# Kernel optimization log

Hardware: AMD Instinct MI355X
Metric: run time of the kernel (lower is better)

Reference implementation:

```python
import jax, jax.numpy as jnp
import numpy as np

NUM_EMBEDDINGS = 1024
EMBEDDING_DIM = 256


def setup_inputs() -> dict:
    key = jax.random.key(0)
    k_in, k_w = jax.random.split(key)
    inputs = jax.random.normal(k_in, (32, EMBEDDING_DIM, 2048), dtype=jnp.float32)
    # nn.Embedding weight initialized uniform in [-1/K, 1/K]
    bound = 1.0 / NUM_EMBEDDINGS
    weight = jax.random.uniform(k_w, (NUM_EMBEDDINGS, EMBEDDING_DIM),
                                dtype=jnp.float32, minval=-bound, maxval=bound)
    return {"inputs": inputs, "weight": weight}


def reference(inputs, weight):
    B, D, T = inputs.shape
    # [B, D, T] -> [B*T, D]
    flat = jnp.transpose(inputs, (0, 2, 1)).reshape(-1, D)
    distances = (jnp.sum(flat * flat, axis=1, keepdims=True)
                 + jnp.sum(weight * weight, axis=1)
                 - 2.0 * flat @ weight.T)  # [N, K]
    encoding_indices = jnp.argmin(distances, axis=1)  # [N]
    # one-hot @ weight is just a gather
    quantized = weight[encoding_indices].reshape(B, T, D)  # [B, T, D]
    quantized = jnp.transpose(quantized, (0, 2, 1))  # [B, D, T]
    # straight-through estimator
    quantized = inputs + jax.lax.stop_gradient(quantized - inputs)
    return quantized, encoding_indices[:, None]
```

## Files before the change

### kernel.cpp

```cpp
#include <hip/hip_runtime.h>


#define VQ_B   32
#define VQ_D   256
#define VQ_T   2048
#define VQ_K   1024

typedef _Float16 f16x8 __attribute__((ext_vector_type(8)));
typedef _Float16 f16x4 __attribute__((ext_vector_type(4)));
typedef float    f32x4 __attribute__((ext_vector_type(4)));

#define GLOAD_LDS16(gaddr, laddr) \
  __builtin_amdgcn_global_load_lds((const __attribute__((address_space(1))) void*)(gaddr), \
                                   (__attribute__((address_space(3))) void*)(laddr), 16, 0, 0)

__global__ __launch_bounds__(256) void vq_wprep_kernel(
    const float* __restrict__ w, float* __restrict__ wnorm,
    _Float16* __restrict__ Wh, _Float16* __restrict__ Wl)
{
    __shared__ double ws_[16][16];
    const int tid = threadIdx.x;
    const int kk  = tid >> 4;
    const int dg  = tid & 15;
    const int k   = blockIdx.x * 16 + kk;
    const float* src = w + (size_t)k * VQ_D + dg * 16;
    double s = 0.0;
    #pragma unroll
    for (int q = 0; q < 4; ++q) {
        float4 v = *(const float4*)(src + q * 4);
        s += (double)v.x * v.x + (double)v.y * v.y
           + (double)v.z * v.z + (double)v.w * v.w;
        const float e4[4] = {v.x, v.y, v.z, v.w};
        f16x4 hv, lv;
        #pragma unroll
        for (int j = 0; j < 4; ++j) {
            const float es = e4[j] * 1024.0f;
            const _Float16 h = (_Float16)es;
            hv[j] = h;
            lv[j] = (_Float16)((es - (float)h) * 16777216.0f);
        }
        *(f16x4*)(Wh + (size_t)k * VQ_D + dg * 16 + q * 4) = hv;
        *(f16x4*)(Wl + (size_t)k * VQ_D + dg * 16 + q * 4) = lv;
    }
    ws_[kk][dg] = s;
    __syncthreads();
    if (dg == 0) {
        double acc = 0.0;
        #pragma unroll
        for (int g = 0; g < 16; ++g) acc += ws_[kk][g];
        wnorm[k] = (float)acc;
    }
}

__global__ __launch_bounds__(256, 2) void vq_mfma_kernel(
    const _Float16* __restrict__ Wh, const _Float16* __restrict__ Wl,
    const float* __restrict__ inp,
    const float* __restrict__ wnorm,
    const float* __restrict__ w,
    float* __restrict__ outq, float* __restrict__ outi)
{
    __shared__ alignas(16) char stg[2][32768];
    __shared__ double xs[2][128];
    const int tid  = threadIdx.x;
    const int lane = tid & 63;
    const int wv   = tid >> 6;
    const int m16  = lane & 15;
    const int quad = lane >> 4;
    const int wm   = wv & 1;
    const int wn   = wv >> 1;
    const int b    = blockIdx.x >> 4;
    const int tt0  = (blockIdx.x & 15) * 128;
    const long bt  = (long)b * VQ_T + tt0;

    const char* gp[8];
    #pragma unroll
    for (int i = 0; i < 8; ++i) {
        if (wv < 2) {
            const int hf = i >> 2, f = i & 3;
            const char* baseW = (const char*)((wv & 1) ? Wl : Wh);
            gp[i] = baseW + (size_t)(hf * 64 + f * 16 + m16) * 512 + quad * 16;
        } else {
            const int r  = (wv - 2) * 16 + i * 2 + (lane >> 5);
            const int sw = ((wv - 2) * 2 + (i >> 2)) * 2;
            gp[i] = (const char*)inp
                  + ((size_t)b * VQ_D + r) * (size_t)(VQ_T * 4)
                  + (size_t)(tt0 * 4)
                  + (size_t)(((lane & 31) ^ sw) * 16);
        }
    }
    auto advance = [&](int q) {
        if ((q & 7) == 7) {
            #pragma unroll
            for (int i = 0; i < 8; ++i)
                gp[i] += (wv < 2) ? (long)(65536 - 448) : (long)(-7) * 262144;
        } else {
            #pragma unroll
            for (int i = 0; i < 8; ++i)
                gp[i] += (wv < 2) ? 64L : 262144L;
        }
    };

    int tsw[4];
    #pragma unroll
    for (int f = 0; f < 4; ++f) {
        const int tl = wn * 64 + f * 16 + m16;
        tsw[f] = (((tl >> 2) ^ (quad * 2)) << 2) | (tl & 3);
    }

    const int xt_t  = tid & 127;
    const int xhalf = tid >> 7;
    double xacc = 0.0;
    float  xnr[4];

    float bestv[4] = {3.0e38f, 3.0e38f, 3.0e38f, 3.0e38f};
    int   besti[4] = {0, 0, 0, 0};
    f32x4 acch[4][4], accl[4][4];

    #pragma unroll
    for (int i = 0; i < 8; ++i)
        GLOAD_LDS16(gp[i], &stg[0][(wv * 8 + i) * 1024]);
    advance(0);

    for (int s = 0; s < 64; ++s) {
        const int cur = s & 1;
        if ((s & 7) == 0) {
            #pragma unroll
            for (int fm = 0; fm < 4; ++fm)
                #pragma unroll
                for (int fn = 0; fn < 4; ++fn) {
                    acch[fm][fn] = (f32x4){0.f, 0.f, 0.f, 0.f};
                    accl[fm][fn] = (f32x4){0.f, 0.f, 0.f, 0.f};
                }
        }
        __syncthreads();
        if (s < 63) {
            #pragma unroll
            for (int i = 0; i < 8; ++i)
                GLOAD_LDS16(gp[i], &stg[cur ^ 1][(wv * 8 + i) * 1024]);
            advance(s + 1);
        }

        const char*  base  = stg[cur];
        const float* xtile = (const float*)(base + 16384);

        f16x8 ah[4], al[4], bh[4], bl[4];
        #pragma unroll
        for (int f = 0; f < 4; ++f) {
            ah[f] = *(const f16x8*)(base + ((wm * 4 + f)) * 1024 + lane * 16);
            al[f] = *(const f16x8*)(base + ((8 + wm * 4 + f)) * 1024 + lane * 16);
        }
        #pragma unroll
        for (int f = 0; f < 4; ++f) {
            f16x8 hv, lv;
            #pragma unroll
            for (int j = 0; j < 8; ++j) {
                const float x = xtile[(quad * 8 + j) * 128 + tsw[f]];
                const _Float16 h = (_Float16)x;
                hv[j] = h;
                lv[j] = (_Float16)((x - (float)h) * 16777216.0f);
            }
            bh[f] = hv; bl[f] = lv;
        }

        #pragma unroll
        for (int fm = 0; fm < 4; ++fm)
            #pragma unroll
            for (int fn = 0; fn < 4; ++fn) {
                acch[fm][fn] = __builtin_amdgcn_mfma_f32_16x16x32_f16(
                    ah[fm], bh[fn], acch[fm][fn], 0, 0, 0);
                accl[fm][fn] = __builtin_amdgcn_mfma_f32_16x16x32_f16(
                    ah[fm], bl[fn], accl[fm][fn], 0, 0, 0);
                accl[fm][fn] = __builtin_amdgcn_mfma_f32_16x16x32_f16(
                    al[fm], bh[fn], accl[fm][fn], 0, 0, 0);
            }

        if (s < 8 && (s >> 2) == xhalf) {
            #pragma unroll
            for (int dd = 0; dd < 32; ++dd) {
                const float x = xtile[dd * 128 +
                    ((((xt_t >> 2) ^ ((dd >> 3) * 2)) << 2) | (xt_t & 3))];
                xacc += (double)x * (double)x;
            }
        }
        if (s == 7) {
            xs[xhalf][xt_t] = xacc;
            __syncthreads();
            #pragma unroll
            for (int fn = 0; fn < 4; ++fn) {
                const int tl = wn * 64 + fn * 16 + m16;
                xnr[fn] = (float)(xs[0][tl] + xs[1][tl]);
            }
        }

        if ((s & 7) == 7) {
            const int k0 = (s >> 3) * 128;
            #pragma unroll
            for (int fm = 0; fm < 4; ++fm) {
                #pragma unroll
                for (int r = 0; r < 4; ++r) {
                    const int kg = k0 + wm * 64 + fm * 16 + quad * 4 + r;
                    const float wnk = wnorm[kg];
                    #pragma unroll
                    for (int fn = 0; fn < 4; ++fn) {
                        const float t1 = xnr[fn] + wnk;
                        const float d2 = (acch[fm][fn][r]
                                          + accl[fm][fn][r] * 5.9604644775390625e-8f)
                                         * 0.001953125f;
                        const float sc = t1 - d2;
                        if (sc < bestv[fn]) { bestv[fn] = sc; besti[fn] = kg; }
                    }
                }
            }
        }
    }

    float rv[4]; int ri[4];
    #pragma unroll
    for (int fn = 0; fn < 4; ++fn) {
        float bv = bestv[fn]; int bi = besti[fn];
        #pragma unroll
        for (int mask = 16; mask <= 32; mask <<= 1) {
            const float ov = __shfl_xor(bv, mask, 64);
            const int   oi = __shfl_xor(bi, mask, 64);
            if (ov < bv || (ov == bv && oi < bi)) { bv = ov; bi = oi; }
        }
        rv[fn] = bv; ri[fn] = bi;
    }

    __syncthreads();
    float* sv = (float*)stg[0];
    int*   si = (int*)(stg[0] + 1024);
    if (quad == 0) {
        #pragma unroll
        for (int fn = 0; fn < 4; ++fn) {
            const int tl = wn * 64 + fn * 16 + m16;
            sv[wm * 128 + tl] = rv[fn];
            si[wm * 128 + tl] = ri[fn];
        }
    }
    __syncthreads();
    if (tid < 128) {
        const float v0 = sv[tid], v1 = sv[128 + tid];
        const int   i0 = si[tid], i1 = si[128 + tid];
        const int   bi = (v1 < v0 || (v1 == v0 && i1 < i0)) ? i1 : i0;
        si[tid] = bi;
        outi[bt + tid] = (float)bi;
    }
    __syncthreads();

    {
        const int t  = tid & 127;
        const int dh = tid >> 7;
        const int bi = si[t];
        const float* wrow = w + (size_t)bi * VQ_D + dh * 128;
        float* obase = outq + ((size_t)b * VQ_D + (size_t)dh * 128) * VQ_T + tt0 + t;
        #pragma unroll 4
        for (int dd = 0; dd < 128; dd += 4) {
            float4 v = *(const float4*)(wrow + dd);
            obase[(size_t)(dd + 0) * VQ_T] = v.x;
            obase[(size_t)(dd + 1) * VQ_T] = v.y;
            obase[(size_t)(dd + 2) * VQ_T] = v.z;
            obase[(size_t)(dd + 3) * VQ_T] = v.w;
        }
    }
}

extern "C" void kernel_launch(void* const* d_in, const int* in_sizes, int n_in,
                              void* d_out, int out_size, void* d_ws, size_t ws_size,
                              hipStream_t stream) {
    const float* inp = (const float*)d_in[0];
    const float* w   = (const float*)d_in[1];
    float* outq  = (float*)d_out;
    float* outi  = outq + (size_t)VQ_B * VQ_D * VQ_T;

    float*    wnorm = (float*)d_ws;
    _Float16* Wh    = (_Float16*)(wnorm + VQ_K);
    _Float16* Wl    = Wh + (size_t)VQ_K * VQ_D;

    vq_wprep_kernel<<<dim3(VQ_K / 16), dim3(256), 0, stream>>>(w, wnorm, Wh, Wl);
    vq_mfma_kernel<<<dim3(VQ_B * (VQ_T / 128)), dim3(256), 0, stream>>>(
        Wh, Wl, inp, wnorm, w, outq, outi);
}
```

Before: 251.8 us.

## Keep pre-split input tile resident in LDS and stream codebook through registers

The input tile for 64 tokens is loaded from global memory once, split into fp16 hi/lo parts and kept resident in LDS, with the token norm computed in the same pass. Before, the fp32 input tile was re-fetched from global memory and re-split on every step for each of the 8 codebook groups. The fp16 codebook is now streamed through registers into LDS with a register prefetch, replacing the async global-to-LDS double buffer. The token tile is halved and the grid doubled, which lowers MFMA reuse per step, doubles total codebook reads from L2 and adds a second barrier per step.

```diff
diff --git a/kernel.cpp b/kernel.cpp
--- a/kernel.cpp
+++ b/kernel.cpp
@@ -9,10 +9,6 @@
 typedef _Float16 f16x8 __attribute__((ext_vector_type(8)));
 typedef _Float16 f16x4 __attribute__((ext_vector_type(4)));
 typedef float    f32x4 __attribute__((ext_vector_type(4)));
-
-#define GLOAD_LDS16(gaddr, laddr) \
-  __builtin_amdgcn_global_load_lds((const __attribute__((address_space(1))) void*)(gaddr), \
-                                   (__attribute__((address_space(3))) void*)(laddr), 16, 0, 0)
 
 __global__ __launch_bounds__(256) void vq_wprep_kernel(
     const float* __restrict__ w, float* __restrict__ wnorm,
@@ -59,8 +55,11 @@
     const float* __restrict__ w,
     float* __restrict__ outq, float* __restrict__ outi)
 {
-    __shared__ alignas(16) char stg[2][32768];
-    __shared__ double xs[2][128];
+    __shared__ alignas(16) char lds[81920];
+    char* Xh = lds;
+    char* Xl = lds + 32768;
+    char* Wb = lds + 65536;
+
     const int tid  = threadIdx.x;
     const int lane = tid & 63;
     const int wv   = tid >> 6;
@@ -68,104 +67,111 @@
     const int quad = lane >> 4;
     const int wm   = wv & 1;
     const int wn   = wv >> 1;
-    const int b    = blockIdx.x >> 4;
-    const int tt0  = (blockIdx.x & 15) * 128;
+    const int b    = blockIdx.x >> 5;
+    const int tt0  = (blockIdx.x & 31) * 64;
     const long bt  = (long)b * VQ_T + tt0;
 
-    const char* gp[8];
-    #pragma unroll
-    for (int i = 0; i < 8; ++i) {
-        if (wv < 2) {
-            const int hf = i >> 2, f = i & 3;
-            const char* baseW = (const char*)((wv & 1) ? Wl : Wh);
-            gp[i] = baseW + (size_t)(hf * 64 + f * 16 + m16) * 512 + quad * 16;
-        } else {
-            const int r  = (wv - 2) * 16 + i * 2 + (lane >> 5);
-            const int sw = ((wv - 2) * 2 + (i >> 2)) * 2;
-            gp[i] = (const char*)inp
-                  + ((size_t)b * VQ_D + r) * (size_t)(VQ_T * 4)
-                  + (size_t)(tt0 * 4)
-                  + (size_t)(((lane & 31) ^ sw) * 16);
-        }
-    }
-    auto advance = [&](int q) {
-        if ((q & 7) == 7) {
-            #pragma unroll
-            for (int i = 0; i < 8; ++i)
-                gp[i] += (wv < 2) ? (long)(65536 - 448) : (long)(-7) * 262144;
-        } else {
-            #pragma unroll
-            for (int i = 0; i < 8; ++i)
-                gp[i] += (wv < 2) ? 64L : 262144L;
-        }
-    };
-
-    int tsw[4];
-    #pragma unroll
-    for (int f = 0; f < 4; ++f) {
-        const int tl = wn * 64 + f * 16 + m16;
-        tsw[f] = (((tl >> 2) ^ (quad * 2)) << 2) | (tl & 3);
-    }
-
-    const int xt_t  = tid & 127;
-    const int xhalf = tid >> 7;
+    const int sel  = tid >> 7;
+    const int r128 = tid & 127;
+    const _Float16* wsrc = (sel ? Wl : Wh) + (size_t)r128 * VQ_D;
+    char* wdst = Wb + (sel * 8 + (r128 >> 6) * 4 + ((r128 >> 4) & 3)) * 1024
+               + (r128 & 15) * 16;
+
+    f16x8 wreg[4];
+    #pragma unroll
+    for (int q = 0; q < 4; ++q)
+        wreg[q] = *(const f16x8*)(wsrc + q * 8);
+
+    const int xt = m16 + wv * 16;
     double xacc = 0.0;
-    float  xnr[4];
-
-    float bestv[4] = {3.0e38f, 3.0e38f, 3.0e38f, 3.0e38f};
-    int   besti[4] = {0, 0, 0, 0};
-    f32x4 acch[4][4], accl[4][4];
-
-    #pragma unroll
-    for (int i = 0; i < 8; ++i)
-        GLOAD_LDS16(gp[i], &stg[0][(wv * 8 + i) * 1024]);
-    advance(0);
+    {
+        float xv[2][8];
+        const float* xp0 = inp + ((size_t)b * VQ_D + quad * 8) * VQ_T + tt0 + xt;
+        #pragma unroll
+        for (int j = 0; j < 8; ++j)
+            xv[0][j] = xp0[(size_t)j * VQ_T];
+        #pragma unroll
+        for (int c = 0; c < 8; ++c) {
+            if (c < 7) {
+                const float* xpn = inp
+                    + ((size_t)b * VQ_D + (c + 1) * 32 + quad * 8) * VQ_T
+                    + tt0 + xt;
+                #pragma unroll
+                for (int j = 0; j < 8; ++j)
+                    xv[(c + 1) & 1][j] = xpn[(size_t)j * VQ_T];
+            }
+            f16x8 hv, lv;
+            #pragma unroll
+            for (int j = 0; j < 8; ++j) {
+                const float x = xv[c & 1][j];
+                xacc += (double)x * (double)x;
+                const _Float16 h = (_Float16)x;
+                hv[j] = h;
+                lv[j] = (_Float16)((x - (float)h) * 16777216.0f);
+            }
+            const int off = ((c * 4 + quad) * 64 + xt) * 16;
+            *(f16x8*)(Xh + off) = hv;
+            *(f16x8*)(Xl + off) = lv;
+        }
+    }
+    xacc += __shfl_xor(xacc, 16, 64);
+    xacc += __shfl_xor(xacc, 32, 64);
+    {
+        float* xns = (float*)Wb;
+        if (quad == 0) xns[xt] = (float)xacc;
+    }
+    __syncthreads();
+    float xnr[2];
+    #pragma unroll
+    for (int f = 0; f < 2; ++f)
+        xnr[f] = ((const float*)Wb)[wn * 32 + f * 16 + m16];
+    __syncthreads();
+
+    float bestv[2] = {3.0e38f, 3.0e38f};
+    int   besti[2] = {0, 0};
+    f32x4 acch[4][2], accl[4][2];
 
     for (int s = 0; s < 64; ++s) {
-        const int cur = s & 1;
-        if ((s & 7) == 0) {
+        const int c = s & 7;
+        #pragma unroll
+        for (int q = 0; q < 4; ++q)
+            *(f16x8*)(wdst + q * 256) = wreg[q];
+        __syncthreads();
+        if (s < 63) {
+            const int s1  = s + 1;
+            const _Float16* src = wsrc
+                + (size_t)((s1 >> 3) * 128) * VQ_D + (s1 & 7) * 32;
+            #pragma unroll
+            for (int q = 0; q < 4; ++q)
+                wreg[q] = *(const f16x8*)(src + q * 8);
+        }
+
+        if (c == 0) {
             #pragma unroll
             for (int fm = 0; fm < 4; ++fm)
                 #pragma unroll
-                for (int fn = 0; fn < 4; ++fn) {
+                for (int fn = 0; fn < 2; ++fn) {
                     acch[fm][fn] = (f32x4){0.f, 0.f, 0.f, 0.f};
                     accl[fm][fn] = (f32x4){0.f, 0.f, 0.f, 0.f};
                 }
         }
-        __syncthreads();
-        if (s < 63) {
-            #pragma unroll
-            for (int i = 0; i < 8; ++i)
-                GLOAD_LDS16(gp[i], &stg[cur ^ 1][(wv * 8 + i) * 1024]);
-            advance(s + 1);
-        }
-
-        const char*  base  = stg[cur];
-        const float* xtile = (const float*)(base + 16384);
-
-        f16x8 ah[4], al[4], bh[4], bl[4];
-        #pragma unroll
-        for (int f = 0; f < 4; ++f) {
-            ah[f] = *(const f16x8*)(base + ((wm * 4 + f)) * 1024 + lane * 16);
-            al[f] = *(const f16x8*)(base + ((8 + wm * 4 + f)) * 1024 + lane * 16);
-        }
-        #pragma unroll
-        for (int f = 0; f < 4; ++f) {
-            f16x8 hv, lv;
-            #pragma unroll
-            for (int j = 0; j < 8; ++j) {
-                const float x = xtile[(quad * 8 + j) * 128 + tsw[f]];
-                const _Float16 h = (_Float16)x;
-                hv[j] = h;
-                lv[j] = (_Float16)((x - (float)h) * 16777216.0f);
-            }
-            bh[f] = hv; bl[f] = lv;
-        }
-
+
+        f16x8 ah[4], al[4], bh[2], bl[2];
+        #pragma unroll
+        for (int fm = 0; fm < 4; ++fm) {
+            ah[fm] = *(const f16x8*)(Wb + (wm * 4 + fm) * 1024 + lane * 16);
+            al[fm] = *(const f16x8*)(Wb + (8 + wm * 4 + fm) * 1024 + lane * 16);
+        }
+        #pragma unroll
+        for (int f = 0; f < 2; ++f) {
+            const int off = ((c * 4 + quad) * 64 + wn * 32 + f * 16 + m16) * 16;
+            bh[f] = *(const f16x8*)(Xh + off);
+            bl[f] = *(const f16x8*)(Xl + off);
+        }
         #pragma unroll
         for (int fm = 0; fm < 4; ++fm)
             #pragma unroll
-            for (int fn = 0; fn < 4; ++fn) {
+            for (int fn = 0; fn < 2; ++fn) {
                 acch[fm][fn] = __builtin_amdgcn_mfma_f32_16x16x32_f16(
                     ah[fm], bh[fn], acch[fm][fn], 0, 0, 0);
                 accl[fm][fn] = __builtin_amdgcn_mfma_f32_16x16x32_f16(
@@ -174,25 +180,7 @@
                     al[fm], bh[fn], accl[fm][fn], 0, 0, 0);
             }
 
-        if (s < 8 && (s >> 2) == xhalf) {
-            #pragma unroll
-            for (int dd = 0; dd < 32; ++dd) {
-                const float x = xtile[dd * 128 +
-                    ((((xt_t >> 2) ^ ((dd >> 3) * 2)) << 2) | (xt_t & 3))];
-                xacc += (double)x * (double)x;
-            }
-        }
-        if (s == 7) {
-            xs[xhalf][xt_t] = xacc;
-            __syncthreads();
-            #pragma unroll
-            for (int fn = 0; fn < 4; ++fn) {
-                const int tl = wn * 64 + fn * 16 + m16;
-                xnr[fn] = (float)(xs[0][tl] + xs[1][tl]);
-            }
-        }
-
-        if ((s & 7) == 7) {
+        if (c == 7) {
             const int k0 = (s >> 3) * 128;
             #pragma unroll
             for (int fm = 0; fm < 4; ++fm) {
@@ -201,7 +189,7 @@
                     const int kg = k0 + wm * 64 + fm * 16 + quad * 4 + r;
                     const float wnk = wnorm[kg];
                     #pragma unroll
-                    for (int fn = 0; fn < 4; ++fn) {
+                    for (int fn = 0; fn < 2; ++fn) {
                         const float t1 = xnr[fn] + wnk;
                         const float d2 = (acch[fm][fn][r]
                                           + accl[fm][fn][r] * 5.9604644775390625e-8f)
@@ -212,11 +200,12 @@
                 }
             }
         }
-    }
-
-    float rv[4]; int ri[4];
-    #pragma unroll
-    for (int fn = 0; fn < 4; ++fn) {
+        __syncthreads();
+    }
+
+    float rv[2]; int ri[2];
+    #pragma unroll
+    for (int fn = 0; fn < 2; ++fn) {
         float bv = bestv[fn]; int bi = besti[fn];
         #pragma unroll
         for (int mask = 16; mask <= 32; mask <<= 1) {
@@ -227,21 +216,20 @@
         rv[fn] = bv; ri[fn] = bi;
     }
 
-    __syncthreads();
-    float* sv = (float*)stg[0];
-    int*   si = (int*)(stg[0] + 1024);
+    float* sv = (float*)lds;
+    int*   si = (int*)(lds + 1024);
     if (quad == 0) {
         #pragma unroll
-        for (int fn = 0; fn < 4; ++fn) {
-            const int tl = wn * 64 + fn * 16 + m16;
-            sv[wm * 128 + tl] = rv[fn];
-            si[wm * 128 + tl] = ri[fn];
-        }
-    }
-    __syncthreads();
-    if (tid < 128) {
-        const float v0 = sv[tid], v1 = sv[128 + tid];
-        const int   i0 = si[tid], i1 = si[128 + tid];
+        for (int fn = 0; fn < 2; ++fn) {
+            const int tl = wn * 32 + fn * 16 + m16;
+            sv[wm * 64 + tl] = rv[fn];
+            si[wm * 64 + tl] = ri[fn];
+        }
+    }
+    __syncthreads();
+    if (tid < 64) {
+        const float v0 = sv[tid], v1 = sv[64 + tid];
+        const int   i0 = si[tid], i1 = si[64 + tid];
         const int   bi = (v1 < v0 || (v1 == v0 && i1 < i0)) ? i1 : i0;
         si[tid] = bi;
         outi[bt + tid] = (float)bi;
@@ -249,13 +237,13 @@
     __syncthreads();
 
     {
-        const int t  = tid & 127;
-        const int dh = tid >> 7;
+        const int t  = tid & 63;
+        const int dq = tid >> 6;
         const int bi = si[t];
-        const float* wrow = w + (size_t)bi * VQ_D + dh * 128;
-        float* obase = outq + ((size_t)b * VQ_D + (size_t)dh * 128) * VQ_T + tt0 + t;
+        const float* wrow = w + (size_t)bi * VQ_D + dq * 64;
+        float* obase = outq + ((size_t)b * VQ_D + (size_t)dq * 64) * VQ_T + tt0 + t;
         #pragma unroll 4
-        for (int dd = 0; dd < 128; dd += 4) {
+        for (int dd = 0; dd < 64; dd += 4) {
             float4 v = *(const float4*)(wrow + dd);
             obase[(size_t)(dd + 0) * VQ_T] = v.x;
             obase[(size_t)(dd + 1) * VQ_T] = v.y;
@@ -278,6 +266,6 @@
     _Float16* Wl    = Wh + (size_t)VQ_K * VQ_D;
 
     vq_wprep_kernel<<<dim3(VQ_K / 16), dim3(256), 0, stream>>>(w, wnorm, Wh, Wl);
-    vq_mfma_kernel<<<dim3(VQ_B * (VQ_T / 128)), dim3(256), 0, stream>>>(
+    vq_mfma_kernel<<<dim3(VQ_B * (VQ_T / 64)), dim3(256), 0, stream>>>(
         Wh, Wl, inp, wnorm, w, outq, outi);
 }
```

Measured after the change: 247.1 us. No clear change (-1.9%).
